# Kernel optimization log

Hardware: AMD Instinct MI355X
Metric: run time of the kernel (lower is better)

## Reference

```python
import jax, jax.numpy as jnp
import numpy as np
from jax import lax

N_DEV = 10

def _branch(inp, w, b, g, bt, m, v):
    # Conv2d(3->4,k3,s1,p1) + BatchNorm2d(eval stats) + ReLU + MaxPool2d(2)
    y = lax.conv_general_dilated(inp, w, (1, 1), ((1, 1), (1, 1)),
                                 dimension_numbers=('NCHW', 'OIHW', 'NCHW'))
    y = y + b[None, :, None, None]
    scale = (g / jnp.sqrt(v + 1e-5))[None, :, None, None]
    y = (y - m[None, :, None, None]) * scale + bt[None, :, None, None]
    y = jnp.maximum(y, 0.0)
    y = lax.reduce_window(y, -jnp.inf, lax.max, (1, 1, 2, 2), (1, 1, 2, 2), 'VALID')
    return y.reshape(y.shape[0], -1)

def _forward(x, conv_w, conv_b, bn_gamma, bn_beta, bn_mean, bn_var,
             cut_w_big, cut_w_small, fc1_w, fc1_b, fc2_w, fc2_b,
             out_w, out_b, b_mat, h_mat, a_mat, indicator, noise):
    zs = []
    for n in range(N_DEV):
        if n <= 1:
            inp = x[:, :, 32 * n:32 * n + 32, :32]
        else:
            r = (16 * (n - 2)) % 64
            c = 32 + 16 * ((n - 2) // 4)
            inp = x[:, :, r:r + 16, c:c + 16]
        flat = _branch(inp, conv_w[n], conv_b[n], bn_gamma[n], bn_beta[n],
                       bn_mean[n], bn_var[n])
        w = cut_w_big[n] if n <= 1 else cut_w_small[n - 2]
        zs.append(flat @ w.T)  # [B, 256]
    z = jnp.stack(zs)                           # [n_dev, B, 256]
    transmit = z * b_mat[:, None, :]            # per-device precoding
    # indicator is one-hot over subcarriers: h_sel[n, j] = h_mat[n, k(j)]
    h_sel = jnp.einsum('jk,nkc->njc', indicator, h_mat)   # [n_dev, 256, 5]
    # h_vec[n, j] = sum(a_mat[j].T @ h_sel[n, j])
    h_vec = jnp.einsum('njc,jcm->nj', h_sel, a_mat)       # [n_dev, 256]
    received = jnp.sum(transmit * h_vec[:, None, :], axis=0)  # [B, 256]
    noise_term = jnp.einsum('jc,jcm->j', noise, a_mat)        # [256]
    received = received + noise_term[None, :]
    h1 = jnp.maximum(received, 0.0)
    h2 = jnp.maximum(h1 @ fc1_w.T + fc1_b, 0.0)
    h3 = jnp.maximum(h2 @ fc2_w.T + fc2_b, 0.0)
    logits = h3 @ out_w.T + out_b
    return jax.nn.log_softmax(logits, axis=1)

def setup_inputs() -> dict:
    key = jax.random.key(0)
    ks = jax.random.split(key, 12)
    B, K, s = 4096, 64, 0.02
    return {
        'x': jax.random.normal(ks[0], (B, 3, 64, 64), jnp.float32),
        'conv_w': jax.random.normal(ks[1], (10, 4, 3, 3, 3), jnp.float32) * s,
        'conv_b': jnp.zeros((10, 4), jnp.float32),
        'bn_gamma': jnp.ones((10, 4), jnp.float32),
        'bn_beta': jnp.zeros((10, 4), jnp.float32),
        'bn_mean': jnp.zeros((10, 4), jnp.float32),
        'bn_var': jnp.ones((10, 4), jnp.float32),
        'cut_w_big': jax.random.normal(ks[2], (2, 256, 1024), jnp.float32) * s,
        'cut_w_small': jax.random.normal(ks[3], (8, 256, 256), jnp.float32) * s,
        'fc1_w': jax.random.normal(ks[4], (128, 256), jnp.float32) * s,
        'fc1_b': jnp.zeros((128,), jnp.float32),
        'fc2_w': jax.random.normal(ks[5], (64, 128), jnp.float32) * s,
        'fc2_b': jnp.zeros((64,), jnp.float32),
        'out_w': jax.random.normal(ks[6], (10, 64), jnp.float32) * s,
        'out_b': jnp.zeros((10,), jnp.float32),
        'b_mat': jax.random.normal(ks[7], (10, 256), jnp.float32) * 0.1,
        'h_mat': jax.random.normal(ks[8], (10, K, 5), jnp.float32),
        'a_mat': jax.random.normal(ks[9], (256, 5, 5), jnp.float32) * 0.1,
        'indicator': jax.nn.one_hot(
            jax.random.randint(ks[10], (256,), 0, K), K, dtype=jnp.float32),
        'noise': jax.random.normal(ks[11], (256, 5), jnp.float32) * 0.1,
    }

def reference(x, conv_w, conv_b, bn_gamma, bn_beta, bn_mean, bn_var,
              cut_w_big, cut_w_small, fc1_w, fc1_b, fc2_w, fc2_b,
              out_w, out_b, b_mat, h_mat, a_mat, indicator, noise):
    return _forward(x, conv_w, conv_b, bn_gamma, bn_beta, bn_mean, bn_var,
                    cut_w_big, cut_w_small, fc1_w, fc1_b, fc2_w, fc2_b,
                    out_w, out_b, b_mat, h_mat, a_mat, indicator, noise)
```

## Files before the change

kernel.cpp:

```cpp
#include <hip/hip_runtime.h>
#include <math.h>

typedef __attribute__((ext_vector_type(8))) short bf16x8;
typedef __attribute__((ext_vector_type(4))) float f32x4;

static __device__ __forceinline__ short f2bf(float f) {
    union { float f; unsigned u; } v; v.f = f;
    unsigned r = v.u + 0x7FFFu + ((v.u >> 16) & 1u);
    return (short)(r >> 16);
}


__global__ __launch_bounds__(256) void k_build_w(
    const float* __restrict__ cut_w_big,
    const float* __restrict__ cut_w_small,
    const float* __restrict__ b_mat,
    const float* __restrict__ h_mat,
    const float* __restrict__ a_mat,
    const float* __restrict__ indicator,
    short* __restrict__ W)
{
    int bx = blockIdx.x;
    int tid0 = bx << 8;
    int j = tid0 >> 12;
    int kbase = tid0 & 4095;
    int n = (kbase < 2048) ? (kbase >> 10) : 2 + ((kbase - 2048) >> 8);

    float arow[5];
#pragma unroll
    for (int c = 0; c < 5; ++c) {
        float s = 0.f;
#pragma unroll
        for (int m = 0; m < 5; ++m) s += a_mat[j * 25 + c * 5 + m];
        arow[c] = s;
    }
    int lane = threadIdx.x & 63;
    float hs = 0.f;
#pragma unroll
    for (int c = 0; c < 5; ++c) hs += h_mat[(n * 64 + lane) * 5 + c] * arow[c];
    float v = indicator[j * 64 + lane] * hs;
#pragma unroll
    for (int off = 32; off >= 1; off >>= 1) v += __shfl_xor(v, off);
    float coeff = b_mat[n * 256 + j] * v;

    int tid = tid0 + threadIdx.x;
    int k = tid & 4095;
    float w;
    if (k < 2048) {
        int nn = k >> 10;
        int r = k & 1023;
        int pos = r >> 2, co = r & 3;
        w = cut_w_big[((nn * 256 + j) << 10) + co * 256 + pos];
    } else {
        int kk2 = k - 2048;
        int nn = kk2 >> 8;
        int r = kk2 & 255;
        int pos = r >> 2, co = r & 3;
        w = cut_w_small[((nn * 256 + j) << 8) + co * 64 + pos];
    }
    W[tid] = f2bf(w * coeff);
}

__global__ __launch_bounds__(256) void k_branch(
    const float* __restrict__ x,
    const float* __restrict__ conv_w,
    const float* __restrict__ conv_b,
    const float* __restrict__ bn_g,
    const float* __restrict__ bn_b,
    const float* __restrict__ bn_m,
    const float* __restrict__ bn_v,
    short* __restrict__ F)
{
    __shared__ float in_s[5184];
    __shared__ float bn_a[4], bn_c[4];
    int t = threadIdx.x;
    int bx = blockIdx.x;

    if (bx < 8192) {
        int n = bx >> 12;
        int b = bx & 4095;
        int r0 = 32 * n;
        for (int i = t; i < 408; i += 256) {
            int ci = i / 136, rem = i % 136;
            int seg = rem / 34, off = rem % 34;
            int addr;
            if (seg == 0)      addr = ci * 1360 + 3 + off;
            else if (seg == 1) addr = ci * 1360 + 33 * 40 + 3 + off;
            else if (seg == 2) addr = ci * 1360 + off * 40 + 3;
            else               addr = ci * 1360 + off * 40 + 36;
            in_s[addr] = 0.f;
        }
        for (int i = t; i < 768; i += 256) {
            int ci = i >> 8, rem = i & 255, yy = rem >> 3, xq = rem & 7;
            float4 v = *(const float4*)(x + ((size_t)(b * 3 + ci) * 64 + r0 + yy) * 64 + xq * 4);
            *(float4*)&in_s[ci * 1360 + (yy + 1) * 40 + 4 + xq * 4] = v;
        }
        if (t < 4) {
            float scale = bn_g[n * 4 + t] * rsqrtf(bn_v[n * 4 + t] + 1e-5f);
            bn_a[t] = scale;
            bn_c[t] = (conv_b[n * 4 + t] - bn_m[n * 4 + t]) * scale + bn_b[n * 4 + t];
        }
        __syncthreads();

        int py = t >> 4, px = t & 15;
        float s[4][4];
#pragma unroll
        for (int a = 0; a < 4; ++a)
#pragma unroll
            for (int p = 0; p < 4; ++p) s[a][p] = 0.f;
        const float* wp = conv_w + n * 108;
#pragma unroll
        for (int ci = 0; ci < 3; ++ci) {
            float wv[16];
            int base = ci * 1360 + (2 * py) * 40 + 3 + 2 * px;
#pragma unroll
            for (int dy = 0; dy < 4; ++dy)
#pragma unroll
                for (int dx = 0; dx < 4; ++dx)
                    wv[dy * 4 + dx] = in_s[base + dy * 40 + dx];
#pragma unroll
            for (int co = 0; co < 4; ++co) {
                const float* kk = wp + co * 27 + ci * 9;
                float k0 = kk[0], k1 = kk[1], k2 = kk[2], k3 = kk[3], k4 = kk[4],
                      k5 = kk[5], k6 = kk[6], k7 = kk[7], k8 = kk[8];
                s[co][0] += wv[0] * k0 + wv[1] * k1 + wv[2] * k2 + wv[4] * k3 + wv[5] * k4 + wv[6] * k5 + wv[8] * k6 + wv[9] * k7 + wv[10] * k8;
                s[co][1] += wv[1] * k0 + wv[2] * k1 + wv[3] * k2 + wv[5] * k3 + wv[6] * k4 + wv[7] * k5 + wv[9] * k6 + wv[10] * k7 + wv[11] * k8;
                s[co][2] += wv[4] * k0 + wv[5] * k1 + wv[6] * k2 + wv[8] * k3 + wv[9] * k4 + wv[10] * k5 + wv[12] * k6 + wv[13] * k7 + wv[14] * k8;
                s[co][3] += wv[5] * k0 + wv[6] * k1 + wv[7] * k2 + wv[9] * k3 + wv[10] * k4 + wv[11] * k5 + wv[13] * k6 + wv[14] * k7 + wv[15] * k8;
            }
        }
        short4 pk;
        {
            float m[4];
#pragma unroll
            for (int co = 0; co < 4; ++co) {
                float a = bn_a[co], c2 = bn_c[co];
                float v0 = fmaxf(s[co][0] * a + c2, 0.f);
                float v1 = fmaxf(s[co][1] * a + c2, 0.f);
                float v2 = fmaxf(s[co][2] * a + c2, 0.f);
                float v3 = fmaxf(s[co][3] * a + c2, 0.f);
                m[co] = fmaxf(fmaxf(v0, v1), fmaxf(v2, v3));
            }
            pk.x = f2bf(m[0]); pk.y = f2bf(m[1]); pk.z = f2bf(m[2]); pk.w = f2bf(m[3]);
        }
        *(short4*)&F[(size_t)b * 4096 + n * 1024 + t * 4] = pk;
    } else {
        int i2 = bx - 8192;
        int n = 2 + (i2 >> 10);
        int g = i2 & 1023;
        int b0 = g * 4;
        int r0 = 16 * ((n - 2) & 3);
        int c0 = 32 + 16 * ((n - 2) >> 2);
        for (int i = t; i < 864; i += 256) {
            int page = i / 72, rem = i % 72;
            int seg = rem / 18, off = rem % 18;
            int addr;
            if (seg == 0)      addr = page * 432 + 3 + off;
            else if (seg == 1) addr = page * 432 + 17 * 24 + 3 + off;
            else if (seg == 2) addr = page * 432 + off * 24 + 3;
            else               addr = page * 432 + off * 24 + 20;
            in_s[addr] = 0.f;
        }
        for (int i = t; i < 768; i += 256) {
            int page = i >> 6, rem = i & 63, yy = rem >> 2, xq = rem & 3;
            int ci = page >> 2, img = page & 3;
            float4 v = *(const float4*)(x + ((size_t)((b0 + img) * 3 + ci) * 64 + r0 + yy) * 64 + c0 + xq * 4);
            *(float4*)&in_s[page * 432 + (yy + 1) * 24 + 4 + xq * 4] = v;
        }
        if (t < 4) {
            float scale = bn_g[n * 4 + t] * rsqrtf(bn_v[n * 4 + t] + 1e-5f);
            bn_a[t] = scale;
            bn_c[t] = (conv_b[n * 4 + t] - bn_m[n * 4 + t]) * scale + bn_b[n * 4 + t];
        }
        __syncthreads();

        int img = t >> 6;
        int pos = t & 63;
        int py = pos >> 3, px = pos & 7;
        float s[4][4];
#pragma unroll
        for (int a = 0; a < 4; ++a)
#pragma unroll
            for (int p = 0; p < 4; ++p) s[a][p] = 0.f;
        const float* wp = conv_w + n * 108;
#pragma unroll
        for (int ci = 0; ci < 3; ++ci) {
            float wv[16];
            int base = (ci * 4 + img) * 432 + (2 * py) * 24 + 3 + 2 * px;
#pragma unroll
            for (int dy = 0; dy < 4; ++dy)
#pragma unroll
                for (int dx = 0; dx < 4; ++dx)
                    wv[dy * 4 + dx] = in_s[base + dy * 24 + dx];
#pragma unroll
            for (int co = 0; co < 4; ++co) {
                const float* kk = wp + co * 27 + ci * 9;
                float k0 = kk[0], k1 = kk[1], k2 = kk[2], k3 = kk[3], k4 = kk[4],
                      k5 = kk[5], k6 = kk[6], k7 = kk[7], k8 = kk[8];
                s[co][0] += wv[0] * k0 + wv[1] * k1 + wv[2] * k2 + wv[4] * k3 + wv[5] * k4 + wv[6] * k5 + wv[8] * k6 + wv[9] * k7 + wv[10] * k8;
                s[co][1] += wv[1] * k0 + wv[2] * k1 + wv[3] * k2 + wv[5] * k3 + wv[6] * k4 + wv[7] * k5 + wv[9] * k6 + wv[10] * k7 + wv[11] * k8;
                s[co][2] += wv[4] * k0 + wv[5] * k1 + wv[6] * k2 + wv[8] * k3 + wv[9] * k4 + wv[10] * k5 + wv[12] * k6 + wv[13] * k7 + wv[14] * k8;
                s[co][3] += wv[5] * k0 + wv[6] * k1 + wv[7] * k2 + wv[9] * k3 + wv[10] * k4 + wv[11] * k5 + wv[13] * k6 + wv[14] * k7 + wv[15] * k8;
            }
        }
        short4 pk;
        {
            float m[4];
#pragma unroll
            for (int co = 0; co < 4; ++co) {
                float a = bn_a[co], c2 = bn_c[co];
                float v0 = fmaxf(s[co][0] * a + c2, 0.f);
                float v1 = fmaxf(s[co][1] * a + c2, 0.f);
                float v2 = fmaxf(s[co][2] * a + c2, 0.f);
                float v3 = fmaxf(s[co][3] * a + c2, 0.f);
                m[co] = fmaxf(fmaxf(v0, v1), fmaxf(v2, v3));
            }
            pk.x = f2bf(m[0]); pk.y = f2bf(m[1]); pk.z = f2bf(m[2]); pk.w = f2bf(m[3]);
        }
        *(short4*)&F[(size_t)(b0 + img) * 4096 + 2048 + (n - 2) * 256 + pos * 4] = pk;
    }
}

__global__ __launch_bounds__(256) void k_gemm(
    const short* __restrict__ F,
    const short* __restrict__ W,
    float* __restrict__ P)
{
    __shared__ short As[128 * 64];
    __shared__ short Bs[128 * 64];
    int bx = blockIdx.x;
    int mt = bx & 31;
    int jt = (bx >> 5) & 1;
    int ks = bx >> 6;
    int t = threadIdx.x;
    int m0 = mt << 7, j0 = jt << 7;

    int lane = t & 63;
    int wave = t >> 6;
    int wm = wave & 1, wn = wave >> 1;
    int l16 = lane & 15, quad = lane >> 4;

    f32x4 acc[4][4];
#pragma unroll
    for (int i = 0; i < 4; ++i)
#pragma unroll
        for (int j = 0; j < 4; ++j) acc[i][j] = (f32x4){0.f, 0.f, 0.f, 0.f};

    for (int it = 0; it < 8; ++it) {
        int k0 = (ks << 9) + (it << 6);
#pragma unroll
        for (int r = 0; r < 4; ++r) {
            int c = (r << 8) + t;
            int row = c >> 3, sgl = c & 7;
            int gsw = sgl ^ (row & 7);
            const short* gpA = F + ((size_t)(m0 + row) << 12) + k0 + (gsw << 3);
            const short* gpB = W + ((size_t)(j0 + row) << 12) + k0 + (gsw << 3);
            __builtin_amdgcn_global_load_lds(
                (const __attribute__((address_space(1))) void*)gpA,
                (__attribute__((address_space(3))) void*)(As + (c << 3)), 16, 0, 0);
            __builtin_amdgcn_global_load_lds(
                (const __attribute__((address_space(1))) void*)gpB,
                (__attribute__((address_space(3))) void*)(Bs + (c << 3)), 16, 0, 0);
        }
        __syncthreads();
#pragma unroll
        for (int ks2 = 0; ks2 < 2; ++ks2) {
            bf16x8 af[4], bfr[4];
#pragma unroll
            for (int mi = 0; mi < 4; ++mi) {
                int row = (wm << 6) + (mi << 4) + l16;
                int q = (ks2 << 2) + quad;
                int sl = q ^ (row & 7);
                af[mi] = *(const bf16x8*)&As[(row << 6) + (sl << 3)];
            }
#pragma unroll
            for (int ni = 0; ni < 4; ++ni) {
                int row = (wn << 6) + (ni << 4) + l16;
                int q = (ks2 << 2) + quad;
                int sl = q ^ (row & 7);
                bfr[ni] = *(const bf16x8*)&Bs[(row << 6) + (sl << 3)];
            }
#pragma unroll
            for (int mi = 0; mi < 4; ++mi)
#pragma unroll
                for (int ni = 0; ni < 4; ++ni)
                    acc[mi][ni] = __builtin_amdgcn_mfma_f32_16x16x32_bf16(
                        af[mi], bfr[ni], acc[mi][ni], 0, 0, 0);
        }
        __syncthreads();
    }

    float* Pp = P + ((size_t)ks << 20);
#pragma unroll
    for (int mi = 0; mi < 4; ++mi)
#pragma unroll
        for (int ni = 0; ni < 4; ++ni) {
            int col = j0 + (wn << 6) + (ni << 4) + l16;
#pragma unroll
            for (int r = 0; r < 4; ++r) {
                int row = m0 + (wm << 6) + (mi << 4) + (quad << 2) + r;
                Pp[(size_t)row * 256 + col] = acc[mi][ni][r];
            }
        }
}

__global__ __launch_bounds__(256) void k_mlp(
    const float* __restrict__ P,
    const float* __restrict__ a_mat,
    const float* __restrict__ noise,
    const float* __restrict__ fc1_w, const float* __restrict__ fc1_b,
    const float* __restrict__ fc2_w, const float* __restrict__ fc2_b,
    const float* __restrict__ out_w, const float* __restrict__ out_b,
    float* __restrict__ out)
{
    __shared__ __align__(16) float Rt[8][260];
    __shared__ __align__(16) float H2[8][132];
    __shared__ __align__(16) float H3[8][68];
    __shared__ float LG[8][12];
    __shared__ float mrow[8], srow[8];
    __shared__ float nts[256];
    int t = threadIdx.x;
    int b0 = blockIdx.x * 8;

    {
        float nt = 0.f;
#pragma unroll
        for (int c = 0; c < 5; ++c) {
            float ar = 0.f;
#pragma unroll
            for (int m = 0; m < 5; ++m) ar += a_mat[t * 25 + c * 5 + m];
            nt += noise[t * 5 + c] * ar;
        }
        nts[t] = nt;
    }
    __syncthreads();

    for (int i = t; i < 512; i += 256) {
        int r = i >> 6;
        int c4 = i & 63;
        size_t base = (size_t)(b0 + r) * 256 + c4 * 4;
        float4 sum = *(const float4*)&nts[c4 * 4];
#pragma unroll
        for (int ks = 0; ks < 8; ++ks) {
            float4 p = *(const float4*)(P + ((size_t)ks << 20) + base);
            sum.x += p.x; sum.y += p.y; sum.z += p.z; sum.w += p.w;
        }
        sum.x = fmaxf(sum.x, 0.f); sum.y = fmaxf(sum.y, 0.f);
        sum.z = fmaxf(sum.z, 0.f); sum.w = fmaxf(sum.w, 0.f);
        *(float4*)&Rt[r][c4 * 4] = sum;
    }
    __syncthreads();

    for (int i = t; i < 1024; i += 256) {
        int r = i & 7, o = i >> 3;
        float s = fc1_b[o];
        const float* wpt = fc1_w + o * 256;
        for (int c = 0; c < 256; c += 4) {
            float4 wv = *(const float4*)(wpt + c);
            float4 rv = *(const float4*)&Rt[r][c];
            s += rv.x * wv.x + rv.y * wv.y + rv.z * wv.z + rv.w * wv.w;
        }
        H2[r][o] = fmaxf(s, 0.f);
    }
    __syncthreads();

    for (int i = t; i < 512; i += 256) {
        int r = i & 7, o = i >> 3;
        float s = fc2_b[o];
        const float* wpt = fc2_w + o * 128;
        for (int c = 0; c < 128; c += 4) {
            float4 wv = *(const float4*)(wpt + c);
            float4 rv = *(const float4*)&H2[r][c];
            s += rv.x * wv.x + rv.y * wv.y + rv.z * wv.z + rv.w * wv.w;
        }
        H3[r][o] = fmaxf(s, 0.f);
    }
    __syncthreads();

    if (t < 80) {
        int r = t & 7, o = t >> 3;
        float s = out_b[o];
        const float* wpt = out_w + o * 64;
        for (int c = 0; c < 64; c += 4) {
            float4 wv = *(const float4*)(wpt + c);
            float4 rv = *(const float4*)&H3[r][c];
            s += rv.x * wv.x + rv.y * wv.y + rv.z * wv.z + rv.w * wv.w;
        }
        LG[r][o] = s;
    }
    __syncthreads();

    if (t < 8) {
        float m = -1e30f;
#pragma unroll
        for (int o = 0; o < 10; ++o) m = fmaxf(m, LG[t][o]);
        float s = 0.f;
#pragma unroll
        for (int o = 0; o < 10; ++o) s += expf(LG[t][o] - m);
        mrow[t] = m;
        srow[t] = logf(s);
    }
    __syncthreads();

    if (t < 80) {
        int r = t & 7, o = t >> 3;
        out[(size_t)(b0 + r) * 10 + o] = LG[r][o] - mrow[r] - srow[r];
    }
}

extern "C" void kernel_launch(void* const* d_in, const int* in_sizes, int n_in,
                              void* d_out, int out_size, void* d_ws, size_t ws_size,
                              hipStream_t stream)
{
    const float* x           = (const float*)d_in[0];
    const float* conv_w      = (const float*)d_in[1];
    const float* conv_b      = (const float*)d_in[2];
    const float* bn_gamma    = (const float*)d_in[3];
    const float* bn_beta     = (const float*)d_in[4];
    const float* bn_mean     = (const float*)d_in[5];
    const float* bn_var      = (const float*)d_in[6];
    const float* cut_w_big   = (const float*)d_in[7];
    const float* cut_w_small = (const float*)d_in[8];
    const float* fc1_w       = (const float*)d_in[9];
    const float* fc1_b       = (const float*)d_in[10];
    const float* fc2_w       = (const float*)d_in[11];
    const float* fc2_b       = (const float*)d_in[12];
    const float* out_w       = (const float*)d_in[13];
    const float* out_b       = (const float*)d_in[14];
    const float* b_mat       = (const float*)d_in[15];
    const float* h_mat       = (const float*)d_in[16];
    const float* a_mat       = (const float*)d_in[17];
    const float* indicator   = (const float*)d_in[18];
    const float* noise       = (const float*)d_in[19];
    float* out = (float*)d_out;

    char* ws = (char*)d_ws;
    short* Fbf = (short*)ws;
    short* Wbf = (short*)(ws + 33554432);
    float* P   = (float*)(ws + 35651584);

    k_build_w<<<4096, 256, 0, stream>>>(cut_w_big, cut_w_small, b_mat, h_mat,
                                        a_mat, indicator, Wbf);
    k_branch<<<16384, 256, 0, stream>>>(x, conv_w, conv_b, bn_gamma, bn_beta,
                                        bn_mean, bn_var, Fbf);
    k_gemm<<<512, 256, 0, stream>>>(Fbf, Wbf, P);
    k_mlp<<<512, 256, 0, stream>>>(P, a_mat, noise, fc1_w, fc1_b, fc2_w, fc2_b,
                                   out_w, out_b, out);
}
```

Measured before the change: 423.2 us.

## Deinterleave conv shared tiles into even/odd planes and split MLP K-loops

The conv branch kernel now stores each input tile in shared memory as separate even-column and odd-column planes. This is meant to cut LDS bank conflicts on the stride-2 pooled window reads and to shrink the shared footprint, which could raise occupancy. In the MLP kernel, each thread now handles one output column for all 8 rows over half (fc1) or a quarter (fc2) of the K dimension, and the partial sums are reduced through shared memory. This lets each weight float4 be reused across 8 rows instead of being reloaded per row, at the cost of extra shared buffers and syncs.

After: 385.3 us. -9.0%, faster.

```diff
diff --git a/kernel.cpp b/kernel.cpp
--- a/kernel.cpp
+++ b/kernel.cpp
@@ -71,7 +71,7 @@
     const float* __restrict__ bn_v,
     short* __restrict__ F)
 {
-    __shared__ float in_s[5184];
+    __shared__ float in_s[4320];
     __shared__ float bn_a[4], bn_c[4];
     int t = threadIdx.x;
     int bx = blockIdx.x;
@@ -80,20 +80,31 @@
         int n = bx >> 12;
         int b = bx & 4095;
         int r0 = 32 * n;
-        for (int i = t; i < 408; i += 256) {
-            int ci = i / 136, rem = i % 136;
-            int seg = rem / 34, off = rem % 34;
+        for (int i = t; i < 504; i += 256) {
             int addr;
-            if (seg == 0)      addr = ci * 1360 + 3 + off;
-            else if (seg == 1) addr = ci * 1360 + 33 * 40 + 3 + off;
-            else if (seg == 2) addr = ci * 1360 + off * 40 + 3;
-            else               addr = ci * 1360 + off * 40 + 36;
+            if (i < 216) {
+                int ci = i / 72, rem = i % 72;
+                int pl = rem / 36, rem2 = rem % 36;
+                int row = (rem2 >= 18) ? 33 : 0;
+                int col = rem2 % 18;
+                addr = ci * 1224 + pl * 612 + row * 18 + col;
+            } else {
+                int jx = i - 216;
+                int ci = jx / 96, rem = jx % 96;
+                int row = rem / 3 + 1, wh = rem % 3;
+                addr = ci * 1224 + row * 18 +
+                       (wh == 0 ? 16 : (wh == 1 ? 612 + 0 : 612 + 17));
+            }
             in_s[addr] = 0.f;
         }
         for (int i = t; i < 768; i += 256) {
             int ci = i >> 8, rem = i & 255, yy = rem >> 3, xq = rem & 7;
             float4 v = *(const float4*)(x + ((size_t)(b * 3 + ci) * 64 + r0 + yy) * 64 + xq * 4);
-            *(float4*)&in_s[ci * 1360 + (yy + 1) * 40 + 4 + xq * 4] = v;
+            int eb = ci * 1224 + (yy + 1) * 18;
+            int ob = eb + 612;
+            *(float2*)&in_s[eb + 2 * xq] = make_float2(v.x, v.z);
+            in_s[ob + 2 * xq + 1] = v.y;
+            in_s[ob + 2 * xq + 2] = v.w;
         }
         if (t < 4) {
             float scale = bn_g[n * 4 + t] * rsqrtf(bn_v[n * 4 + t] + 1e-5f);
@@ -112,12 +123,16 @@
 #pragma unroll
         for (int ci = 0; ci < 3; ++ci) {
             float wv[16];
-            int base = ci * 1360 + (2 * py) * 40 + 3 + 2 * px;
-#pragma unroll
-            for (int dy = 0; dy < 4; ++dy)
-#pragma unroll
-                for (int dx = 0; dx < 4; ++dx)
-                    wv[dy * 4 + dx] = in_s[base + dy * 40 + dx];
+#pragma unroll
+            for (int dy = 0; dy < 4; ++dy) {
+                int rowb = ci * 1224 + (2 * py + dy) * 18 + px;
+                float e0 = in_s[rowb];
+                float e1 = in_s[rowb + 1];
+                float o0 = in_s[rowb + 612];
+                float o1 = in_s[rowb + 613];
+                wv[dy * 4 + 0] = o0; wv[dy * 4 + 1] = e0;
+                wv[dy * 4 + 2] = o1; wv[dy * 4 + 3] = e1;
+            }
 #pragma unroll
             for (int co = 0; co < 4; ++co) {
                 const float* kk = wp + co * 27 + ci * 9;
@@ -152,20 +167,30 @@
         int r0 = 16 * ((n - 2) & 3);
         int c0 = 32 + 16 * ((n - 2) >> 2);
         for (int i = t; i < 864; i += 256) {
-            int page = i / 72, rem = i % 72;
-            int seg = rem / 18, off = rem % 18;
             int addr;
-            if (seg == 0)      addr = page * 432 + 3 + off;
-            else if (seg == 1) addr = page * 432 + 17 * 24 + 3 + off;
-            else if (seg == 2) addr = page * 432 + off * 24 + 3;
-            else               addr = page * 432 + off * 24 + 20;
+            if (i < 480) {
+                int page = i / 40, rem = i % 40;
+                int pl = rem / 20, rem2 = rem % 20;
+                int row = (rem2 >= 10) ? 17 : 0;
+                int col = rem2 % 10;
+                addr = page * 360 + pl * 180 + row * 10 + col;
+            } else {
+                int jx = i - 480;
+                int page = jx / 32, rem = jx % 32;
+                int row = (rem >> 1) + 1, wh = rem & 1;
+                addr = page * 360 + row * 10 + (wh ? 180 + 0 : 8);
+            }
             in_s[addr] = 0.f;
         }
         for (int i = t; i < 768; i += 256) {
             int page = i >> 6, rem = i & 63, yy = rem >> 2, xq = rem & 3;
             int ci = page >> 2, img = page & 3;
             float4 v = *(const float4*)(x + ((size_t)((b0 + img) * 3 + ci) * 64 + r0 + yy) * 64 + c0 + xq * 4);
-            *(float4*)&in_s[page * 432 + (yy + 1) * 24 + 4 + xq * 4] = v;
+            int eb = page * 360 + (yy + 1) * 10;
+            int ob = eb + 180;
+            *(float2*)&in_s[eb + 2 * xq] = make_float2(v.x, v.z);
+            in_s[ob + 2 * xq + 1] = v.y;
+            in_s[ob + 2 * xq + 2] = v.w;
         }
         if (t < 4) {
             float scale = bn_g[n * 4 + t] * rsqrtf(bn_v[n * 4 + t] + 1e-5f);
@@ -186,12 +211,17 @@
 #pragma unroll
         for (int ci = 0; ci < 3; ++ci) {
             float wv[16];
-            int base = (ci * 4 + img) * 432 + (2 * py) * 24 + 3 + 2 * px;
-#pragma unroll
-            for (int dy = 0; dy < 4; ++dy)
-#pragma unroll
-                for (int dx = 0; dx < 4; ++dx)
-                    wv[dy * 4 + dx] = in_s[base + dy * 24 + dx];
+            int pageb = (ci * 4 + img) * 360;
+#pragma unroll
+            for (int dy = 0; dy < 4; ++dy) {
+                int rowb = pageb + (2 * py + dy) * 10 + px;
+                float e0 = in_s[rowb];
+                float e1 = in_s[rowb + 1];
+                float o0 = in_s[rowb + 180];
+                float o1 = in_s[rowb + 181];
+                wv[dy * 4 + 0] = o0; wv[dy * 4 + 1] = e0;
+                wv[dy * 4 + 2] = o1; wv[dy * 4 + 3] = e1;
+            }
 #pragma unroll
             for (int co = 0; co < 4; ++co) {
                 const float* kk = wp + co * 27 + ci * 9;
@@ -314,7 +344,9 @@
     float* __restrict__ out)
 {
     __shared__ __align__(16) float Rt[8][260];
+    __shared__ float P1[2][8][132];
     __shared__ __align__(16) float H2[8][132];
+    __shared__ float P2[4][8][68];
     __shared__ __align__(16) float H3[8][68];
     __shared__ float LG[8][12];
     __shared__ float mrow[8], srow[8];
@@ -351,29 +383,54 @@
     }
     __syncthreads();
 
+    {
+        int o = t & 127, h = t >> 7;
+        float acc[8];
+#pragma unroll
+        for (int r = 0; r < 8; ++r) acc[r] = 0.f;
+        const float* wr = fc1_w + o * 256 + h * 128;
+        for (int c = 0; c < 128; c += 4) {
+            float4 wv = *(const float4*)(wr + c);
+#pragma unroll
+            for (int r = 0; r < 8; ++r) {
+                float4 rv = *(const float4*)&Rt[r][h * 128 + c];
+                acc[r] += rv.x * wv.x + rv.y * wv.y + rv.z * wv.z + rv.w * wv.w;
+            }
+        }
+#pragma unroll
+        for (int r = 0; r < 8; ++r) P1[h][r][o] = acc[r];
+    }
+    __syncthreads();
+
     for (int i = t; i < 1024; i += 256) {
-        int r = i & 7, o = i >> 3;
-        float s = fc1_b[o];
-        const float* wpt = fc1_w + o * 256;
-        for (int c = 0; c < 256; c += 4) {
-            float4 wv = *(const float4*)(wpt + c);
-            float4 rv = *(const float4*)&Rt[r][c];
-            s += rv.x * wv.x + rv.y * wv.y + rv.z * wv.z + rv.w * wv.w;
-        }
-        H2[r][o] = fmaxf(s, 0.f);
+        int r = i >> 7, o = i & 127;
+        H2[r][o] = fmaxf(P1[0][r][o] + P1[1][r][o] + fc1_b[o], 0.f);
+    }
+    __syncthreads();
+
+    {
+        int o = t & 63, q = t >> 6;
+        float acc[8];
+#pragma unroll
+        for (int r = 0; r < 8; ++r) acc[r] = 0.f;
+        const float* wr = fc2_w + o * 128 + q * 32;
+        for (int c = 0; c < 32; c += 4) {
+            float4 wv = *(const float4*)(wr + c);
+#pragma unroll
+            for (int r = 0; r < 8; ++r) {
+                float4 rv = *(const float4*)&H2[r][q * 32 + c];
+                acc[r] += rv.x * wv.x + rv.y * wv.y + rv.z * wv.z + rv.w * wv.w;
+            }
+        }
+#pragma unroll
+        for (int r = 0; r < 8; ++r) P2[q][r][o] = acc[r];
     }
     __syncthreads();
 
     for (int i = t; i < 512; i += 256) {
-        int r = i & 7, o = i >> 3;
-        float s = fc2_b[o];
-        const float* wpt = fc2_w + o * 128;
-        for (int c = 0; c < 128; c += 4) {
-            float4 wv = *(const float4*)(wpt + c);
-            float4 rv = *(const float4*)&H2[r][c];
-            s += rv.x * wv.x + rv.y * wv.y + rv.z * wv.z + rv.w * wv.w;
-        }
-        H3[r][o] = fmaxf(s, 0.f);
+        int r = i >> 6, o = i & 63;
+        H3[r][o] = fmaxf(P2[0][r][o] + P2[1][r][o] + P2[2][r][o] + P2[3][r][o]
+                         + fc2_b[o], 0.f);
     }
     __syncthreads();
 
```
